# Optimization experiments

Hardware: AMD Instinct MI355X
Metric: run time of the kernel (lower is better)

## Reference

```python
import jax, jax.numpy as jnp
import numpy as np

B, N, D, O, L = 16, 2000, 128, 64, 3  # batch, n_nodes, hidden_dim, output_dim, n_layers


def _init(key, shape, fan_in):
    return jax.random.normal(key, shape, jnp.float32) / np.sqrt(fan_in).astype(np.float32)


def setup_inputs() -> dict:
    key = jax.random.key(0)
    ks = jax.random.split(key, 8)
    return {
        "coords": jax.random.normal(ks[0], (B, N, 2), jnp.float32),
        "enc_w0": _init(ks[1], (2, D), 2),
        "enc_b0": jnp.zeros((D,), jnp.float32),
        "enc_w1": _init(ks[2], (D, D), D),
        "enc_b1": jnp.zeros((D,), jnp.float32),
        "gat_W": _init(ks[3], (L, D, D), D),      # per-layer GAT projection (no bias)
        "gat_a1": _init(ks[4], (L, D), 2 * D),    # first half of attention vector a
        "gat_a2": _init(ks[5], (L, D), 2 * D),    # second half of attention vector a
        "proj_w": _init(ks[6], (D, O), D),
        "proj_b": jnp.zeros((O,), jnp.float32),
    }


def _leaky(x):
    return jnp.where(x >= 0, x, 0.2 * x)  # LeakyReLU(0.2)


def reference(coords, enc_w0, enc_b0, enc_w1, enc_b1, gat_W, gat_a1, gat_a2, proj_w, proj_b):
    # node encoder: Linear -> ReLU -> Linear
    h = jax.nn.relu(coords @ enc_w0 + enc_b0) @ enc_w1 + enc_b1  # [B,N,D]
    n_layers = gat_W.shape[0]
    for l in range(n_layers):
        Wh = h @ gat_W[l]                      # [B,N,D]
        # additive GAT attention: e_ij = leakyrelu(a1.Wh_i + a2.Wh_j)
        # (equivalent to a([Wh_i || Wh_j]) without materializing N*N*2D tensor)
        e1 = Wh @ gat_a1[l]                    # [B,N]
        e2 = Wh @ gat_a2[l]                    # [B,N]
        e = _leaky(e1[:, :, None] + e2[:, None, :])  # [B,N,N]
        # adj is all-ones in forward() so the masked_fill is a no-op
        att = jax.nn.softmax(e, axis=-1)       # [B,N,N]; dropout is identity (eval)
        h = jax.nn.relu(att @ Wh)              # [B,N,D]
    return h @ proj_w + proj_b                 # [B,N,O]
```

## Files before the change

### kernel.cpp

```cpp
#include <hip/hip_runtime.h>
#include <hip/hip_bf16.h>

using bf16 = __hip_bfloat16;

#define BATCH 16
#define NNODE 2000
#define DIM   128
#define ODIM  64
#define NLAYER 3
#define BN    (BATCH*NNODE)
#define NP1   (NNODE+1)
#define CHK   125
#define CKS   16

#define OFF_COORDS 0
#define OFF_EW0    64000
#define OFF_EB0    64256
#define OFF_EW1    64384
#define OFF_EB1    80768
#define OFF_GW     80896
#define OFF_GA1    130048
#define OFF_GA2    130432
#define OFF_PW     130816
#define OFF_PB     139008
#define CVT_TOT    139072

#define PK_GAT(l)  (32768 + (l)*32768)
#define PK_PROJ    131072
#define PK_TOT     147456

typedef __attribute__((ext_vector_type(8))) short bf16x8;
typedef __attribute__((ext_vector_type(4))) float f32x4;

__device__ __forceinline__ unsigned short f2bf(float f){
    union { float f; unsigned u; } x; x.f = f;
    unsigned r = (x.u + 0x7FFFu + ((x.u >> 16) & 1u)) >> 16;
    return (unsigned short)r;
}
__device__ __forceinline__ float bf2f(unsigned short h){
    union { unsigned u; float f; } x; x.u = ((unsigned)h) << 16;
    return x.f;
}
__device__ __forceinline__ unsigned ordu(float f){
    union { float f; unsigned u; } x; x.f = f;
    return (x.u & 0x80000000u) ? ~x.u : (x.u | 0x80000000u);
}
__device__ __forceinline__ float iordu(unsigned u){
    union { unsigned u; float f; } x;
    x.u = (u & 0x80000000u) ? (u ^ 0x80000000u) : ~u;
    return x.f;
}

struct InPtrs { const void* p[10]; };

__global__ void convert_all_k(InPtrs in, float* __restrict__ dst, float* __restrict__ flag)
{
    __shared__ int scnt[256];
    const unsigned short* raw = (const unsigned short*)in.p[0];
    int t = threadIdx.x, c = 0;
    for (int k = t; k < 2048; k += 256){
        unsigned short u = raw[2*k];
        int e = (u >> 7) & 0xFF;
        if (e >= 100 && e <= 140) ++c;
    }
    scnt[t] = c;
    __syncthreads();
    for (int s = 128; s; s >>= 1){ if (t < s) scnt[t] += scnt[t+s]; __syncthreads(); }
    const bool isbf16 = (scnt[0] >= 1800);
    if (blockIdx.x == 0 && t == 0) flag[0] = isbf16 ? 1.0f : 0.0f;

    const int off[11] = {OFF_COORDS,OFF_EW0,OFF_EB0,OFF_EW1,OFF_EB1,
                         OFF_GW,OFF_GA1,OFF_GA2,OFF_PW,OFF_PB,CVT_TOT};
    int i = blockIdx.x*256 + t;
    if (i >= CVT_TOT) return;
    int seg = 0;
    #pragma unroll
    for (int s = 1; s < 10; ++s) if (i >= off[s]) seg = s;
    int li = i - off[seg];
    if (isbf16) dst[i] = __bfloat162float(((const bf16*)in.p[seg])[li]);
    else        dst[i] = ((const float*)in.p[seg])[li];
}

__global__ __launch_bounds__(256) void prep_k(const float* __restrict__ cvt,
                                              unsigned short* __restrict__ pk,
                                              float* __restrict__ wa)
{
    const int mi = blockIdx.x, t = threadIdx.x;
    if (mi < 3){
        const float* W; unsigned short* dst; int N;
        if (mi == 0)      { W = cvt + OFF_GW + 1*DIM*DIM;  dst = pk + PK_GAT(1); N = 128; }
        else if (mi == 1) { W = cvt + OFF_GW + 2*DIM*DIM;  dst = pk + PK_GAT(2); N = 128; }
        else              { W = cvt + OFF_PW;              dst = pk + PK_PROJ;   N = 64;  }
        const int tot = 128*N;
        unsigned short* dh = dst;
        unsigned short* dl = dst + tot;
        for (int e = t; e < tot; e += 256){
            int col = e >> 7, k = e & 127;
            float v = W[k*N + col];
            unsigned short hb = f2bf(v);
            unsigned short lb = f2bf(v - bf2f(hb));
            dh[e] = hb;
            dl[e] = lb;
        }
    } else {
        for (int idx = t; idx < 3*256; idx += 256){
            const int l = idx >> 8, rem = idx & 255, half = rem >> 7, r = rem & 127;
            const float* W  = cvt + OFF_GW + l*DIM*DIM;
            const float* av = cvt + (half ? OFF_GA2 : OFF_GA1) + l*DIM;
            float s = 0.f;
            for (int c2 = 0; c2 < 128; ++c2) s = fmaf(W[r*128 + c2], av[c2], s);
            wa[l*256 + half*128 + r] = s;
        }
    }
}

__global__ __launch_bounds__(128) void prep2_k(const float* __restrict__ cvt,
    unsigned short* __restrict__ pk, const float* __restrict__ wa,
    float* __restrict__ u12, float* __restrict__ bfuse, float* __restrict__ su)
{
    const int b = blockIdx.x, t = threadIdx.x;
    const float* w1 = cvt + OFF_EW1;
    const float* W0 = cvt + OFF_GW;
    if (b < 128){
        float acc = 0.f;
        for (int d = 0; d < 128; ++d) acc = fmaf(w1[b*DIM + d], W0[d*DIM + t], acc);
        unsigned short hb = f2bf(acc), lb = f2bf(acc - bf2f(hb));
        unsigned short* dst = pk + PK_GAT(0);
        dst[t*128 + b]         = hb;
        dst[16384 + t*128 + b] = lb;
    } else if (b == 128){
        const float* b1 = cvt + OFF_EB1;
        float acc = 0.f;
        for (int d = 0; d < 128; ++d) acc = fmaf(b1[d], W0[d*DIM + t], acc);
        bfuse[t] = acc;
        if (t < 2){
            float s = 0.f;
            for (int d = 0; d < 128; ++d) s = fmaf(b1[d], wa[t*128 + d], s);
            su[t] = s;
        }
    } else {
        float a1 = 0.f, a2 = 0.f;
        for (int d = 0; d < 128; ++d){
            float w = w1[t*DIM + d];
            a1 = fmaf(w, wa[d],       a1);
            a2 = fmaf(w, wa[128 + d], a2);
        }
        u12[t]       = a1;
        u12[128 + t] = a2;
    }
}


__global__ __launch_bounds__(256) void gat0mfma_k(const float* __restrict__ cvt,
    const unsigned short* __restrict__ pk, const float* __restrict__ u12,
    const float* __restrict__ su, const float* __restrict__ bfuse,
    float* __restrict__ Wh, float* __restrict__ e1p, float* __restrict__ e2p)
{
    __shared__ unsigned short sAh[64*128], sAl[64*128];
    const int t = threadIdx.x, r0 = blockIdx.x*64;
    const int wv = t >> 6, l = t & 63, lc = l & 15, lk = l >> 4;
    const unsigned short* ph = pk;
    const unsigned short* pl = pk + 16384;
    bf16x8 bh[2][4], bl[2][4];
    #pragma unroll
    for (int cg = 0; cg < 2; ++cg){
        const int col = wv*32 + cg*16 + lc;
        #pragma unroll
        for (int kc = 0; kc < 4; ++kc){
            const int k0 = kc*32 + lk*8;
            bh[cg][kc] = *(const bf16x8*)&ph[col*128 + k0];
            bl[cg][kc] = *(const bf16x8*)&pl[col*128 + k0];
        }
    }
    const int row = t >> 2, g = t & 3;
    const float* coords = cvt + OFF_COORDS;
    const float* w0  = cvt + OFF_EW0;
    const float* b0v = cvt + OFF_EB0;
    const int node = r0 + row;
    const float c0 = coords[2*node], c1 = coords[2*node+1];
    char* shb = (char*)sAh; char* slb = (char*)sAl;
    const int swz = (row & 7) << 4;
    float e1 = 0.f, e2 = 0.f;
    #pragma unroll
    for (int i = 0; i < 8; ++i){
        const int ch = g + i*4, k0 = ch*4;
        float4 wa0 = *(const float4*)&w0[k0];
        float4 wb0 = *(const float4*)&w0[DIM + k0];
        float4 bq  = *(const float4*)&b0v[k0];
        float4 v;
        v.x = fmaf(c0, wa0.x, fmaf(c1, wb0.x, bq.x)); v.x = v.x > 0.f ? v.x : 0.f;
        v.y = fmaf(c0, wa0.y, fmaf(c1, wb0.y, bq.y)); v.y = v.y > 0.f ? v.y : 0.f;
        v.z = fmaf(c0, wa0.z, fmaf(c1, wb0.z, bq.z)); v.z = v.z > 0.f ? v.z : 0.f;
        v.w = fmaf(c0, wa0.w, fmaf(c1, wb0.w, bq.w)); v.w = v.w > 0.f ? v.w : 0.f;
        float4 q1 = *(const float4*)&u12[k0];
        float4 q2 = *(const float4*)&u12[128 + k0];
        e1 = fmaf(v.x,q1.x, fmaf(v.y,q1.y, fmaf(v.z,q1.z, fmaf(v.w,q1.w, e1))));
        e2 = fmaf(v.x,q2.x, fmaf(v.y,q2.y, fmaf(v.z,q2.z, fmaf(v.w,q2.w, e2))));
        ushort4 hq, lq;
        hq.x = f2bf(v.x); lq.x = f2bf(v.x - bf2f(hq.x));
        hq.y = f2bf(v.y); lq.y = f2bf(v.y - bf2f(hq.y));
        hq.z = f2bf(v.z); lq.z = f2bf(v.z - bf2f(hq.z));
        hq.w = f2bf(v.w); lq.w = f2bf(v.w - bf2f(hq.w));
        const int bo = (ch*8) ^ swz;
        *(ushort4*)(shb + row*256 + bo) = hq;
        *(ushort4*)(slb + row*256 + bo) = lq;
    }
    e1 += __shfl_xor(e1, 1); e1 += __shfl_xor(e1, 2);
    e2 += __shfl_xor(e2, 1); e2 += __shfl_xor(e2, 2);
    if (g == 0){ e1p[r0 + row] = e1 + su[0]; e2p[r0 + row] = e2 + su[1]; }
    __syncthreads();
    f32x4 acc[4][2] = {};
    #pragma unroll
    for (int m = 0; m < 4; ++m){
        const int ar = m*16 + lc, asw = (ar & 7) << 4;
        #pragma unroll
        for (int kc = 0; kc < 4; ++kc){
            const int bo = (kc*64 + lk*16) ^ asw;
            bf16x8 ah = *(bf16x8*)(shb + ar*256 + bo);
            bf16x8 al = *(bf16x8*)(slb + ar*256 + bo);
            #pragma unroll
            for (int cg = 0; cg < 2; ++cg){
                acc[m][cg] = __builtin_amdgcn_mfma_f32_16x16x32_bf16(ah, bh[cg][kc], acc[m][cg], 0, 0, 0);
                acc[m][cg] = __builtin_amdgcn_mfma_f32_16x16x32_bf16(ah, bl[cg][kc], acc[m][cg], 0, 0, 0);
                acc[m][cg] = __builtin_amdgcn_mfma_f32_16x16x32_bf16(al, bh[cg][kc], acc[m][cg], 0, 0, 0);
            }
        }
    }
    #pragma unroll
    for (int m = 0; m < 4; ++m){
        const int rg = r0 + m*16 + lk*4;
        #pragma unroll
        for (int cg = 0; cg < 2; ++cg){
            const int col = wv*32 + cg*16 + lc;
            const float bb = bfuse[col];
            #pragma unroll
            for (int j = 0; j < 4; ++j) Wh[(size_t)(rg+j)*DIM + col] = acc[m][cg][j] + bb;
        }
    }
}

__global__ __launch_bounds__(256) void gatmfma_k(const float* __restrict__ A,
    const unsigned short* __restrict__ pk, const float* __restrict__ wa,
    float* __restrict__ Wh, float* __restrict__ e1p, float* __restrict__ e2p)
{
    __shared__ unsigned short sAh[64*128], sAl[64*128];
    const int t = threadIdx.x, r0 = blockIdx.x*64;
    const int wv = t >> 6, l = t & 63, lc = l & 15, lk = l >> 4;
    const unsigned short* ph = pk;
    const unsigned short* pl = pk + 16384;
    bf16x8 bh[2][4], bl[2][4];
    #pragma unroll
    for (int cg = 0; cg < 2; ++cg){
        const int col = wv*32 + cg*16 + lc;
        #pragma unroll
        for (int kc = 0; kc < 4; ++kc){
            const int k0 = kc*32 + lk*8;
            bh[cg][kc] = *(const bf16x8*)&ph[col*128 + k0];
            bl[cg][kc] = *(const bf16x8*)&pl[col*128 + k0];
        }
    }
    const int row = t >> 2, g = t & 3;
    const float* Ar = A + (size_t)(r0 + row)*DIM;
    char* shb = (char*)sAh; char* slb = (char*)sAl;
    const int swz = (row & 7) << 4;
    float e1 = 0.f, e2 = 0.f;
    #pragma unroll
    for (int i = 0; i < 8; ++i){
        const int ch = g + i*4;
        float4 a  = *(const float4*)&Ar[ch*4];
        float4 u1 = *(const float4*)&wa[ch*4];
        float4 u2 = *(const float4*)&wa[128 + ch*4];
        e1 = fmaf(a.x,u1.x, fmaf(a.y,u1.y, fmaf(a.z,u1.z, fmaf(a.w,u1.w, e1))));
        e2 = fmaf(a.x,u2.x, fmaf(a.y,u2.y, fmaf(a.z,u2.z, fmaf(a.w,u2.w, e2))));
        ushort4 hq, lq;
        hq.x = f2bf(a.x); lq.x = f2bf(a.x - bf2f(hq.x));
        hq.y = f2bf(a.y); lq.y = f2bf(a.y - bf2f(hq.y));
        hq.z = f2bf(a.z); lq.z = f2bf(a.z - bf2f(hq.z));
        hq.w = f2bf(a.w); lq.w = f2bf(a.w - bf2f(hq.w));
        const int bo = (ch*8) ^ swz;
        *(ushort4*)(shb + row*256 + bo) = hq;
        *(ushort4*)(slb + row*256 + bo) = lq;
    }
    e1 += __shfl_xor(e1, 1); e1 += __shfl_xor(e1, 2);
    e2 += __shfl_xor(e2, 1); e2 += __shfl_xor(e2, 2);
    if (g == 0){ e1p[r0 + row] = e1; e2p[r0 + row] = e2; }
    __syncthreads();
    f32x4 acc[4][2] = {};
    #pragma unroll
    for (int m = 0; m < 4; ++m){
        const int ar = m*16 + lc, asw = (ar & 7) << 4;
        #pragma unroll
        for (int kc = 0; kc < 4; ++kc){
            const int bo = (kc*64 + lk*16) ^ asw;
            bf16x8 ah = *(bf16x8*)(shb + ar*256 + bo);
            bf16x8 al = *(bf16x8*)(slb + ar*256 + bo);
            #pragma unroll
            for (int cg = 0; cg < 2; ++cg){
                acc[m][cg] = __builtin_amdgcn_mfma_f32_16x16x32_bf16(ah, bh[cg][kc], acc[m][cg], 0, 0, 0);
                acc[m][cg] = __builtin_amdgcn_mfma_f32_16x16x32_bf16(ah, bl[cg][kc], acc[m][cg], 0, 0, 0);
                acc[m][cg] = __builtin_amdgcn_mfma_f32_16x16x32_bf16(al, bh[cg][kc], acc[m][cg], 0, 0, 0);
            }
        }
    }
    #pragma unroll
    for (int m = 0; m < 4; ++m){
        const int rg = r0 + m*16 + lk*4;
        #pragma unroll
        for (int cg = 0; cg < 2; ++cg){
            const int col = wv*32 + cg*16 + lc;
            #pragma unroll
            for (int j = 0; j < 4; ++j) Wh[(size_t)(rg+j)*DIM + col] = acc[m][cg][j];
        }
    }
}

__global__ __launch_bounds__(256) void projmfma_k(const float* __restrict__ A,
    const unsigned short* __restrict__ pk, const float* __restrict__ bias,
    void* __restrict__ outp, const float* __restrict__ flag)
{
    __shared__ unsigned short sAh[64*128], sAl[64*128];
    const int t = threadIdx.x, r0 = blockIdx.x*64;
    const int wv = t >> 6, l = t & 63, lc = l & 15, lk = l >> 4;
    const unsigned short* ph = pk;
    const unsigned short* pl = pk + 8192;
    bf16x8 bh[4], bl[4];
    const int col = wv*16 + lc;
    #pragma unroll
    for (int kc = 0; kc < 4; ++kc){
        const int k0 = kc*32 + lk*8;
        bh[kc] = *(const bf16x8*)&ph[col*128 + k0];
        bl[kc] = *(const bf16x8*)&pl[col*128 + k0];
    }
    const int row = t >> 2, g = t & 3;
    const float* Ar = A + (size_t)(r0 + row)*DIM;
    char* shb = (char*)sAh; char* slb = (char*)sAl;
    const int swz = (row & 7) << 4;
    #pragma unroll
    for (int i = 0; i < 8; ++i){
        const int ch = g + i*4;
        float4 a = *(const float4*)&Ar[ch*4];
        ushort4 hq, lq;
        hq.x = f2bf(a.x); lq.x = f2bf(a.x - bf2f(hq.x));
        hq.y = f2bf(a.y); lq.y = f2bf(a.y - bf2f(hq.y));
        hq.z = f2bf(a.z); lq.z = f2bf(a.z - bf2f(hq.z));
        hq.w = f2bf(a.w); lq.w = f2bf(a.w - bf2f(hq.w));
        const int bo = (ch*8) ^ swz;
        *(ushort4*)(shb + row*256 + bo) = hq;
        *(ushort4*)(slb + row*256 + bo) = lq;
    }
    __syncthreads();
    f32x4 acc[4] = {};
    #pragma unroll
    for (int m = 0; m < 4; ++m){
        const int ar = m*16 + lc, asw = (ar & 7) << 4;
        #pragma unroll
        for (int kc = 0; kc < 4; ++kc){
            const int bo = (kc*64 + lk*16) ^ asw;
            bf16x8 ah = *(bf16x8*)(shb + ar*256 + bo);
            bf16x8 al = *(bf16x8*)(slb + ar*256 + bo);
            acc[m] = __builtin_amdgcn_mfma_f32_16x16x32_bf16(ah, bh[kc], acc[m], 0, 0, 0);
            acc[m] = __builtin_amdgcn_mfma_f32_16x16x32_bf16(ah, bl[kc], acc[m], 0, 0, 0);
            acc[m] = __builtin_amdgcn_mfma_f32_16x16x32_bf16(al, bh[kc], acc[m], 0, 0, 0);
        }
    }
    const float bb = bias[col];
    const bool isbf = (flag[0] != 0.0f);
    #pragma unroll
    for (int m = 0; m < 4; ++m){
        const int rg = r0 + m*16 + lk*4;
        #pragma unroll
        for (int j = 0; j < 4; ++j){
            float v = acc[m][j] + bb;
            size_t p = (size_t)(rg+j)*ODIM + col;
            if (isbf) ((bf16*)outp)[p] = __float2bfloat16(v);
            else      ((float*)outp)[p] = v;
        }
    }
}

#define WAVE_FENCE() __asm__ volatile("" ::: "memory")
__global__ void sort_k(const float* __restrict__ e2p, float* __restrict__ e2s, int* __restrict__ sidx,
                       float* __restrict__ wp, float* __restrict__ wn, float* __restrict__ e2m)
{
    __shared__ unsigned long long kv[2048];
    const int b = blockIdx.x, t = threadIdx.x;
    for (int i = t; i < 2048; i += 1024)
        kv[i] = (i < NNODE) ? (((unsigned long long)ordu(e2p[b*NNODE + i]) << 32) | (unsigned)i)
                            : 0xFFFFFFFFFFFFFFFFull;
    __syncthreads();

    #pragma unroll 1
    for (int size = 2; size <= 128; size <<= 1){
        #pragma unroll 1
        for (int stride = size >> 1; stride > 0; stride >>= 1){
            int i = 2*t - (t & (stride-1));
            int j = i + stride;
            bool asc = ((i & size) == 0);
            unsigned long long ki = kv[i], kj = kv[j];
            bool sw = asc ? (ki > kj) : (ki < kj);
            if (sw){ kv[i] = kj; kv[j] = ki; }
            WAVE_FENCE();
        }
    }
    __syncthreads();

    #pragma unroll 1
    for (int size = 256; size <= 2048; size <<= 1){
        #pragma unroll 1
        for (int stride = size >> 1; stride >= 128; stride >>= 1){
            int i = 2*t - (t & (stride-1));
            int j = i + stride;
            bool asc = ((i & size) == 0);
            unsigned long long ki = kv[i], kj = kv[j];
            bool sw = asc ? (ki > kj) : (ki < kj);
            if (sw){ kv[i] = kj; kv[j] = ki; }
            __syncthreads();
        }
        #pragma unroll 1
        for (int stride = 64; stride > 0; stride >>= 1){
            int i = 2*t - (t & (stride-1));
            int j = i + stride;
            bool asc = ((i & size) == 0);
            unsigned long long ki = kv[i], kj = kv[j];
            bool sw = asc ? (ki > kj) : (ki < kj);
            if (sw){ kv[i] = kj; kv[j] = ki; }
            WAVE_FENCE();
        }
        __syncthreads();
    }

    const float mx = iordu((unsigned)(kv[NNODE-1] >> 32));
    for (int i = t; i < NNODE; i += 1024){
        unsigned long long key = kv[i];
        float val = iordu((unsigned)(key >> 32));
        e2s [b*NNODE+i] = val;
        sidx[b*NNODE+i] = (int)(key & 0xFFFFFFFFull);
        wp  [b*NNODE+i] = __expf(val - mx);
        wn  [b*NNODE+i] = __expf(0.2f*(val - mx));
    }
    if (t == 0) e2m[b] = mx;
}

__global__ void passA_k(const float* __restrict__ Wh, const int* __restrict__ sidx,
    const float* __restrict__ wp, const float* __restrict__ wn,
    float* __restrict__ chunkP, float* __restrict__ chunkN,
    float* __restrict__ schunkP, float* __restrict__ schunkN)
{
    const int b = blockIdx.x / CHK, c = blockIdx.x % CHK, d = threadIdx.x;
    const int base = b*NNODE;
    float sp=0.f, sn=0.f, ssp=0.f, ssn=0.f;
    #pragma unroll 4
    for (int r = c*CKS; r < c*CKS + CKS; ++r){
        int j = sidx[base + r];
        float whv = Wh[((size_t)base + j)*DIM + d];
        float wpv = wp[base + r], wnv = wn[base + r];
        sp = fmaf(wpv, whv, sp);  sn = fmaf(wnv, whv, sn);
        ssp += wpv;  ssn += wnv;
    }
    const int idx = b*CHK + c;
    chunkP[idx*DIM + d] = sp;
    chunkN[idx*DIM + d] = sn;
    if (d == 0){ schunkP[idx] = ssp; schunkN[idx] = ssn; }
}

__global__ __launch_bounds__(256) void passB_k(
    const float* __restrict__ chunkP, const float* __restrict__ chunkN,
    const float* __restrict__ schunkP, const float* __restrict__ schunkN,
    float* __restrict__ offP, float* __restrict__ offN,
    float* __restrict__ soffP, float* __restrict__ soffN)
{
    const int b = blockIdx.x, tid = threadIdx.x;
    const bool doP = (blockIdx.y == 0);
    const float* chunk  = doP ? chunkP  : chunkN;
    const float* schunk = doP ? schunkP : schunkN;
    float* off  = doP ? offP  : offN;
    float* soff = doP ? soffP : soffN;

    if (tid < 128){
        const int d = tid;
        float acc = 0.f, v[25];
        #pragma unroll
        for (int t = 0; t < 5; ++t){
            const int c0 = doP ? (4-t)*25 : t*25;
            #pragma unroll
            for (int k = 0; k < 25; ++k) v[k] = chunk[(b*CHK + c0 + k)*DIM + d];
            if (doP){
                #pragma unroll
                for (int k = 24; k >= 0; --k){ off[(b*CHK + c0 + k)*DIM + d] = acc; acc += v[k]; }
            } else {
                #pragma unroll
                for (int k = 0; k < 25; ++k){ off[(b*CHK + c0 + k)*DIM + d] = acc; acc += v[k]; }
            }
        }
    } else if (tid == 128){
        float sacc = 0.f, sv[25];
        #pragma unroll
        for (int t = 0; t < 5; ++t){
            const int c0 = doP ? (4-t)*25 : t*25;
            #pragma unroll
            for (int k = 0; k < 25; ++k) sv[k] = schunk[b*CHK + c0 + k];
            if (doP){
                #pragma unroll
                for (int k = 24; k >= 0; --k){ soff[b*CHK + c0 + k] = sacc; sacc += sv[k]; }
            } else {
                #pragma unroll
                for (int k = 0; k < 25; ++k){ soff[b*CHK + c0 + k] = sacc; sacc += sv[k]; }
            }
        }
    }
}

__global__ void passC_k(const float* __restrict__ Wh, const int* __restrict__ sidx,
    const float* __restrict__ wp, const float* __restrict__ wn,
    const float* __restrict__ offP, const float* __restrict__ offN,
    const float* __restrict__ soffP, const float* __restrict__ soffN,
    float* __restrict__ Ppos, float* __restrict__ Pneg,
    float* __restrict__ pposs, float* __restrict__ pnegs)
{
    const int b = blockIdx.x / CHK, c = blockIdx.x % CHK, d = threadIdx.x;
    const int base = b*NNODE;
    const size_t pb = (size_t)b*NP1;
    const int idx = b*CHK + c;
    const int r0 = c*CKS, r1 = r0 + CKS;

    if (c == CHK-1){
        Ppos[(pb + NNODE)*DIM + d] = 0.f;
        if (d == 0) pposs[pb + NNODE] = 0.f;
    }
    float pr = offP[idx*DIM + d], spr = soffP[idx];
    for (int r = r1-1; r >= r0; --r){
        int j = sidx[base + r];
        float whv = Wh[((size_t)base + j)*DIM + d];
        float wpv = wp[base + r];
        pr  = fmaf(wpv, whv, pr);
        spr += wpv;
        Ppos[(pb + r)*DIM + d] = pr;
        if (d == 0) pposs[pb + r] = spr;
    }
    float nr = offN[idx*DIM + d], snr = soffN[idx];
    for (int r = r0; r < r1; ++r){
        int j = sidx[base + r];
        float whv = Wh[((size_t)base + j)*DIM + d];
        float wnv = wn[base + r];
        Pneg[(pb + r)*DIM + d] = nr;
        if (d == 0) pnegs[pb + r] = snr;
        nr  = fmaf(wnv, whv, nr);
        snr += wnv;
    }
    if (c == CHK-1){
        Pneg[(pb + NNODE)*DIM + d] = nr;
        if (d == 0) pnegs[pb + NNODE] = snr;
    }
}

__global__ __launch_bounds__(128) void out16_k(const float* __restrict__ e1p,
    const float* __restrict__ e2s, const float* __restrict__ e2m,
    const float* __restrict__ Ppos, const float* __restrict__ Pneg,
    const float* __restrict__ pposs, const float* __restrict__ pnegs, float* __restrict__ h)
{
    __shared__ int   slo[CKS];
    __shared__ float sps[CKS], sns[CKS];
    const int b = blockIdx.x / CHK, c = blockIdx.x % CHK, d = threadIdx.x;
    const int base = b*NNODE, r0 = c*CKS;
    const size_t pb = (size_t)b*NP1;

    if (d < CKS){
        int row = base + r0 + d;
        float e1v = e1p[row];
        float s = e1v + e2m[b];
        float m = (s >= 0.f) ? s : 0.2f*s;
        sps[d] = __expf(s - m);
        sns[d] = __expf(0.2f*s - m);
        const float* es = e2s + base;
        float tt = -e1v;
        int lo = 0, hi = NNODE;
        while (lo < hi){ int mid = (lo+hi) >> 1; if (es[mid] < tt) lo = mid+1; else hi = mid; }
        slo[d] = lo;
    }
    __syncthreads();
    #pragma unroll 4
    for (int k = 0; k < CKS; ++k){
        int row = base + r0 + k;
        size_t kb = pb + slo[k];
        float numer = sps[k]*Ppos[kb*DIM + d] + sns[k]*Pneg[kb*DIM + d];
        float Z     = sps[k]*pposs[kb]        + sns[k]*pnegs[kb];
        float q = numer / Z;
        h[(size_t)row*DIM + d] = (q > 0.f) ? q : ((q == q) ? 0.f : q);
    }
}

extern "C" void kernel_launch(void* const* d_in, const int* in_sizes, int n_in,
                              void* d_out, int out_size, void* d_ws, size_t ws_size,
                              hipStream_t stream)
{
    (void)in_sizes; (void)n_in; (void)out_size; (void)ws_size;

    float* f = (float*)d_ws;
    float* flag    = f;  f += 4;
    float* cvt     = f;  f += CVT_TOT;
    float* h       = f;  f += (size_t)BN*DIM;
    float* Wh      = f;  f += (size_t)BN*DIM;
    float* Ppos    = f;  f += (size_t)BATCH*NP1*DIM;
    float* Pneg    = f;  f += (size_t)BATCH*NP1*DIM;
    float* chunkP  = f;  f += BATCH*CHK*DIM;
    float* chunkN  = f;  f += BATCH*CHK*DIM;
    float* offP    = f;  f += BATCH*CHK*DIM;
    float* offN    = f;  f += BATCH*CHK*DIM;
    float* schunkP = f;  f += BATCH*CHK;
    float* schunkN = f;  f += BATCH*CHK;
    float* soffP   = f;  f += BATCH*CHK;
    float* soffN   = f;  f += BATCH*CHK;
    float* e1p     = f;  f += BN;
    float* e2p     = f;  f += BN;
    float* e2s     = f;  f += BN;
    float* wp      = f;  f += BN;
    float* wn      = f;  f += BN;
    float* pposs   = f;  f += BATCH*NP1;
    float* pnegs   = f;  f += BATCH*NP1;
    float* e2m     = f;  f += 16;
    int*   sidx    = (int*)f;
    unsigned short* pk = (unsigned short*)(sidx + BN);
    float* wa      = (float*)(pk + PK_TOT);
    float* u12     = wa + 768;
    float* bfuse   = u12 + 256;
    float* su      = bfuse + 128;

    InPtrs ip;
    for (int i = 0; i < 10; ++i) ip.p[i] = d_in[i];
    convert_all_k<<<(CVT_TOT+255)/256, 256, 0, stream>>>(ip, cvt, flag);

    prep_k<<<4, 256, 0, stream>>>(cvt, pk, wa);
    prep2_k<<<130, 128, 0, stream>>>(cvt, pk, wa, u12, bfuse, su);

    for (int l = 0; l < NLAYER; ++l){
        if (l == 0)
            gat0mfma_k<<<BN/64, 256, 0, stream>>>(cvt, pk + PK_GAT(0), u12, su, bfuse,
                                                  Wh, e1p, e2p);
        else
            gatmfma_k<<<BN/64, 256, 0, stream>>>(h, pk + PK_GAT(l), wa + l*256, Wh, e1p, e2p);
        sort_k<<<BATCH, 1024, 0, stream>>>(e2p, e2s, sidx, wp, wn, e2m);
        passA_k<<<BATCH*CHK, DIM, 0, stream>>>(Wh, sidx, wp, wn, chunkP, chunkN, schunkP, schunkN);
        passB_k<<<dim3(BATCH, 2), 256, 0, stream>>>(chunkP, chunkN, schunkP, schunkN,
                                                    offP, offN, soffP, soffN);
        passC_k<<<BATCH*CHK, DIM, 0, stream>>>(Wh, sidx, wp, wn, offP, offN, soffP, soffN,
                                               Ppos, Pneg, pposs, pnegs);
        out16_k<<<BATCH*CHK, DIM, 0, stream>>>(e1p, e2s, e2m, Ppos, Pneg, pposs, pnegs, h);
    }

    projmfma_k<<<BN/64, 256, 0, stream>>>(h, pk + PK_PROJ, cvt + OFF_PB, d_out, flag);
}
```

Measured before the change: 301.9 us.

## Merge chunk-sum and local prefix passes, apply chunk offsets in output kernel

The chunked prefix-sum scheme previously read the gathered Wh rows twice, once in passA for chunk totals and again in passC for the offset-adjusted prefixes. Now a single pass writes chunk-local prefix sums along with the chunk totals. The output kernel adds the cross-chunk offset from passB at lookup time. This drops one kernel launch per layer and one full gather over Wh, at the cost of two extra offset reads per output row in the final kernel.

```diff
diff --git a/kernel.cpp b/kernel.cpp
--- a/kernel.cpp
+++ b/kernel.cpp
@@ -441,26 +441,52 @@
     if (t == 0) e2m[b] = mx;
 }
 
-__global__ void passA_k(const float* __restrict__ Wh, const int* __restrict__ sidx,
+__global__ void passAC_k(const float* __restrict__ Wh, const int* __restrict__ sidx,
     const float* __restrict__ wp, const float* __restrict__ wn,
+    float* __restrict__ localP, float* __restrict__ localN,
+    float* __restrict__ lposs, float* __restrict__ lnegs,
     float* __restrict__ chunkP, float* __restrict__ chunkN,
     float* __restrict__ schunkP, float* __restrict__ schunkN)
 {
     const int b = blockIdx.x / CHK, c = blockIdx.x % CHK, d = threadIdx.x;
     const int base = b*NNODE;
-    float sp=0.f, sn=0.f, ssp=0.f, ssn=0.f;
-    #pragma unroll 4
-    for (int r = c*CKS; r < c*CKS + CKS; ++r){
+    const size_t pb = (size_t)b*NP1;
+    const int idx = b*CHK + c;
+    const int r0 = c*CKS, r1 = r0 + CKS;
+
+    if (c == CHK-1){
+        localP[(pb + NNODE)*DIM + d] = 0.f;
+        if (d == 0) lposs[pb + NNODE] = 0.f;
+    }
+    float pr = 0.f, spr = 0.f;
+    for (int r = r1-1; r >= r0; --r){
         int j = sidx[base + r];
         float whv = Wh[((size_t)base + j)*DIM + d];
-        float wpv = wp[base + r], wnv = wn[base + r];
-        sp = fmaf(wpv, whv, sp);  sn = fmaf(wnv, whv, sn);
-        ssp += wpv;  ssn += wnv;
-    }
-    const int idx = b*CHK + c;
-    chunkP[idx*DIM + d] = sp;
-    chunkN[idx*DIM + d] = sn;
-    if (d == 0){ schunkP[idx] = ssp; schunkN[idx] = ssn; }
+        float wpv = wp[base + r];
+        pr  = fmaf(wpv, whv, pr);
+        spr += wpv;
+        localP[(pb + r)*DIM + d] = pr;
+        if (d == 0) lposs[pb + r] = spr;
+    }
+    chunkP[idx*DIM + d] = pr;
+    if (d == 0) schunkP[idx] = spr;
+
+    float nr = 0.f, snr = 0.f;
+    for (int r = r0; r < r1; ++r){
+        int j = sidx[base + r];
+        float whv = Wh[((size_t)base + j)*DIM + d];
+        float wnv = wn[base + r];
+        localN[(pb + r)*DIM + d] = nr;
+        if (d == 0) lnegs[pb + r] = snr;
+        nr  = fmaf(wnv, whv, nr);
+        snr += wnv;
+    }
+    if (c == CHK-1){
+        localN[(pb + NNODE)*DIM + d] = nr;
+        if (d == 0) lnegs[pb + NNODE] = snr;
+    }
+    chunkN[idx*DIM + d] = nr;
+    if (d == 0) schunkN[idx] = snr;
 }
 
 __global__ __launch_bounds__(256) void passB_k(
@@ -510,53 +536,13 @@
     }
 }
 
-__global__ void passC_k(const float* __restrict__ Wh, const int* __restrict__ sidx,
-    const float* __restrict__ wp, const float* __restrict__ wn,
+__global__ __launch_bounds__(128) void out16f_k(const float* __restrict__ e1p,
+    const float* __restrict__ e2s, const float* __restrict__ e2m,
+    const float* __restrict__ localP, const float* __restrict__ localN,
+    const float* __restrict__ lposs, const float* __restrict__ lnegs,
     const float* __restrict__ offP, const float* __restrict__ offN,
     const float* __restrict__ soffP, const float* __restrict__ soffN,
-    float* __restrict__ Ppos, float* __restrict__ Pneg,
-    float* __restrict__ pposs, float* __restrict__ pnegs)
-{
-    const int b = blockIdx.x / CHK, c = blockIdx.x % CHK, d = threadIdx.x;
-    const int base = b*NNODE;
-    const size_t pb = (size_t)b*NP1;
-    const int idx = b*CHK + c;
-    const int r0 = c*CKS, r1 = r0 + CKS;
-
-    if (c == CHK-1){
-        Ppos[(pb + NNODE)*DIM + d] = 0.f;
-        if (d == 0) pposs[pb + NNODE] = 0.f;
-    }
-    float pr = offP[idx*DIM + d], spr = soffP[idx];
-    for (int r = r1-1; r >= r0; --r){
-        int j = sidx[base + r];
-        float whv = Wh[((size_t)base + j)*DIM + d];
-        float wpv = wp[base + r];
-        pr  = fmaf(wpv, whv, pr);
-        spr += wpv;
-        Ppos[(pb + r)*DIM + d] = pr;
-        if (d == 0) pposs[pb + r] = spr;
-    }
-    float nr = offN[idx*DIM + d], snr = soffN[idx];
-    for (int r = r0; r < r1; ++r){
-        int j = sidx[base + r];
-        float whv = Wh[((size_t)base + j)*DIM + d];
-        float wnv = wn[base + r];
-        Pneg[(pb + r)*DIM + d] = nr;
-        if (d == 0) pnegs[pb + r] = snr;
-        nr  = fmaf(wnv, whv, nr);
-        snr += wnv;
-    }
-    if (c == CHK-1){
-        Pneg[(pb + NNODE)*DIM + d] = nr;
-        if (d == 0) pnegs[pb + NNODE] = snr;
-    }
-}
-
-__global__ __launch_bounds__(128) void out16_k(const float* __restrict__ e1p,
-    const float* __restrict__ e2s, const float* __restrict__ e2m,
-    const float* __restrict__ Ppos, const float* __restrict__ Pneg,
-    const float* __restrict__ pposs, const float* __restrict__ pnegs, float* __restrict__ h)
+    float* __restrict__ h)
 {
     __shared__ int   slo[CKS];
     __shared__ float sps[CKS], sns[CKS];
@@ -581,9 +567,14 @@
     #pragma unroll 4
     for (int k = 0; k < CKS; ++k){
         int row = base + r0 + k;
-        size_t kb = pb + slo[k];
-        float numer = sps[k]*Ppos[kb*DIM + d] + sns[k]*Pneg[kb*DIM + d];
-        float Z     = sps[k]*pposs[kb]        + sns[k]*pnegs[kb];
+        int lo = slo[k];
+        int cl = lo >> 4; if (cl > CHK-1) cl = CHK-1;
+        size_t kb = pb + lo;
+        int ob = b*CHK + cl;
+        float pP = localP[kb*DIM + d] + offP[(size_t)ob*DIM + d];
+        float pN = localN[kb*DIM + d] + offN[(size_t)ob*DIM + d];
+        float numer = sps[k]*pP + sns[k]*pN;
+        float Z     = sps[k]*(lposs[kb] + soffP[ob]) + sns[k]*(lnegs[kb] + soffN[ob]);
         float q = numer / Z;
         h[(size_t)row*DIM + d] = (q > 0.f) ? q : ((q == q) ? 0.f : q);
     }
@@ -639,12 +630,12 @@
         else
             gatmfma_k<<<BN/64, 256, 0, stream>>>(h, pk + PK_GAT(l), wa + l*256, Wh, e1p, e2p);
         sort_k<<<BATCH, 1024, 0, stream>>>(e2p, e2s, sidx, wp, wn, e2m);
-        passA_k<<<BATCH*CHK, DIM, 0, stream>>>(Wh, sidx, wp, wn, chunkP, chunkN, schunkP, schunkN);
+        passAC_k<<<BATCH*CHK, DIM, 0, stream>>>(Wh, sidx, wp, wn, Ppos, Pneg, pposs, pnegs,
+                                                chunkP, chunkN, schunkP, schunkN);
         passB_k<<<dim3(BATCH, 2), 256, 0, stream>>>(chunkP, chunkN, schunkP, schunkN,
                                                     offP, offN, soffP, soffN);
-        passC_k<<<BATCH*CHK, DIM, 0, stream>>>(Wh, sidx, wp, wn, offP, offN, soffP, soffN,
-                                               Ppos, Pneg, pposs, pnegs);
-        out16_k<<<BATCH*CHK, DIM, 0, stream>>>(e1p, e2s, e2m, Ppos, Pneg, pposs, pnegs, h);
+        out16f_k<<<BATCH*CHK, DIM, 0, stream>>>(e1p, e2s, e2m, Ppos, Pneg, pposs, pnegs,
+                                                offP, offN, soffP, soffN, h);
     }
 
     projmfma_k<<<BN/64, 256, 0, stream>>>(h, pk + PK_PROJ, cvt + OFF_PB, d_out, flag);
```

New measurement: 294.8 us. 2.3% less time.

## Bucket query rows by split point and fuse prefix scan with attention output

Applied to the files above, without the earlier changes.

The sort kernel now also computes each query row's split point and exp scale factors, then counting-sorts rows into buckets keyed by split index. A fused output kernel recomputes chunk offsets directly, walks each chunk's sorted keys in reverse, and writes outputs for rows whose split falls there. This removes the full Ppos/Pneg prefix arrays (16×2001×128×2 floats) and two kernel launches per layer. In exchange, each block redundantly sums up to 125 chunk partials, and per-row work is imbalanced across blocks because bucket sizes vary.

```diff
diff --git a/kernel.cpp b/kernel.cpp
--- a/kernel.cpp
+++ b/kernel.cpp
@@ -12,6 +12,7 @@
 #define NP1   (NNODE+1)
 #define CHK   125
 #define CKS   16
+#define NOFF  2002
 
 #define OFF_COORDS 0
 #define OFF_EW0    64000
@@ -379,10 +380,14 @@
 }
 
 #define WAVE_FENCE() __asm__ volatile("" ::: "memory")
-__global__ void sort_k(const float* __restrict__ e2p, float* __restrict__ e2s, int* __restrict__ sidx,
-                       float* __restrict__ wp, float* __restrict__ wn, float* __restrict__ e2m)
+__global__ void sortE_k(const float* __restrict__ e2p, const float* __restrict__ e1p,
+    int* __restrict__ sidx, float* __restrict__ wp, float* __restrict__ wn,
+    float* __restrict__ sps, float* __restrict__ sns,
+    int* __restrict__ bucketRow, int* __restrict__ bucketOff)
 {
     __shared__ unsigned long long kv[2048];
+    __shared__ int cnt[NOFF];
+    __shared__ int ofs[NOFF];
     const int b = blockIdx.x, t = threadIdx.x;
     for (int i = t; i < 2048; i += 1024)
         kv[i] = (i < NNODE) ? (((unsigned long long)ordu(e2p[b*NNODE + i]) << 32) | (unsigned)i)
@@ -433,15 +438,65 @@
     for (int i = t; i < NNODE; i += 1024){
         unsigned long long key = kv[i];
         float val = iordu((unsigned)(key >> 32));
-        e2s [b*NNODE+i] = val;
         sidx[b*NNODE+i] = (int)(key & 0xFFFFFFFFull);
         wp  [b*NNODE+i] = __expf(val - mx);
         wn  [b*NNODE+i] = __expf(0.2f*(val - mx));
     }
-    if (t == 0) e2m[b] = mx;
-}
-
-__global__ void passA_k(const float* __restrict__ Wh, const int* __restrict__ sidx,
+    for (int i = t; i < NOFF; i += 1024) cnt[i] = 0;
+    __syncthreads();
+
+    int loA[2] = {-1, -1};
+    #pragma unroll
+    for (int q = 0; q < 2; ++q){
+        const int i = t + q*1024;
+        if (i < NNODE){
+            float e1v = e1p[b*NNODE + i];
+            float s = e1v + mx;
+            float m = (s >= 0.f) ? s : 0.2f*s;
+            sps[b*NNODE + i] = __expf(s - m);
+            sns[b*NNODE + i] = __expf(0.2f*s - m);
+            unsigned tt = ordu(-e1v);
+            int lo = 0, hi = NNODE;
+            while (lo < hi){
+                int mid = (lo + hi) >> 1;
+                if ((unsigned)(kv[mid] >> 32) < tt) lo = mid + 1; else hi = mid;
+            }
+            loA[q] = lo;
+            atomicAdd(&cnt[lo], 1);
+        }
+    }
+    __syncthreads();
+
+    if (t < 64){
+        const int b0 = t*32;
+        int s = 0;
+        for (int k = 0; k < 32; ++k){ int id = b0+k; if (id < NOFF) s += cnt[id]; }
+        int inc = s;
+        #pragma unroll
+        for (int d2 = 1; d2 < 64; d2 <<= 1){
+            int v = __shfl_up(inc, d2);
+            if (t >= d2) inc += v;
+        }
+        int run = inc - s;
+        for (int k = 0; k < 32; ++k){ int id = b0+k; if (id < NOFF){ ofs[id] = run; run += cnt[id]; } }
+    }
+    __syncthreads();
+    for (int i = t; i < NOFF; i += 1024){
+        bucketOff[b*NOFF + i] = ofs[i];
+        cnt[i] = ofs[i];
+    }
+    __syncthreads();
+    #pragma unroll
+    for (int q = 0; q < 2; ++q){
+        const int i = t + q*1024;
+        if (i < NNODE){
+            int pos = atomicAdd(&cnt[loA[q]], 1);
+            bucketRow[b*NNODE + pos] = i;
+        }
+    }
+}
+
+__global__ void chunkSums_k(const float* __restrict__ Wh, const int* __restrict__ sidx,
     const float* __restrict__ wp, const float* __restrict__ wn,
     float* __restrict__ chunkP, float* __restrict__ chunkN,
     float* __restrict__ schunkP, float* __restrict__ schunkN)
@@ -463,129 +518,70 @@
     if (d == 0){ schunkP[idx] = ssp; schunkN[idx] = ssn; }
 }
 
-__global__ __launch_bounds__(256) void passB_k(
+__global__ __launch_bounds__(128) void outFused_k(const float* __restrict__ Wh,
+    const int* __restrict__ sidx, const float* __restrict__ wp, const float* __restrict__ wn,
     const float* __restrict__ chunkP, const float* __restrict__ chunkN,
     const float* __restrict__ schunkP, const float* __restrict__ schunkN,
-    float* __restrict__ offP, float* __restrict__ offN,
-    float* __restrict__ soffP, float* __restrict__ soffN)
-{
-    const int b = blockIdx.x, tid = threadIdx.x;
-    const bool doP = (blockIdx.y == 0);
-    const float* chunk  = doP ? chunkP  : chunkN;
-    const float* schunk = doP ? schunkP : schunkN;
-    float* off  = doP ? offP  : offN;
-    float* soff = doP ? soffP : soffN;
-
-    if (tid < 128){
-        const int d = tid;
-        float acc = 0.f, v[25];
-        #pragma unroll
-        for (int t = 0; t < 5; ++t){
-            const int c0 = doP ? (4-t)*25 : t*25;
-            #pragma unroll
-            for (int k = 0; k < 25; ++k) v[k] = chunk[(b*CHK + c0 + k)*DIM + d];
-            if (doP){
-                #pragma unroll
-                for (int k = 24; k >= 0; --k){ off[(b*CHK + c0 + k)*DIM + d] = acc; acc += v[k]; }
-            } else {
-                #pragma unroll
-                for (int k = 0; k < 25; ++k){ off[(b*CHK + c0 + k)*DIM + d] = acc; acc += v[k]; }
-            }
-        }
-    } else if (tid == 128){
-        float sacc = 0.f, sv[25];
-        #pragma unroll
-        for (int t = 0; t < 5; ++t){
-            const int c0 = doP ? (4-t)*25 : t*25;
-            #pragma unroll
-            for (int k = 0; k < 25; ++k) sv[k] = schunk[b*CHK + c0 + k];
-            if (doP){
-                #pragma unroll
-                for (int k = 24; k >= 0; --k){ soff[b*CHK + c0 + k] = sacc; sacc += sv[k]; }
-            } else {
-                #pragma unroll
-                for (int k = 0; k < 25; ++k){ soff[b*CHK + c0 + k] = sacc; sacc += sv[k]; }
-            }
-        }
-    }
-}
-
-__global__ void passC_k(const float* __restrict__ Wh, const int* __restrict__ sidx,
-    const float* __restrict__ wp, const float* __restrict__ wn,
-    const float* __restrict__ offP, const float* __restrict__ offN,
-    const float* __restrict__ soffP, const float* __restrict__ soffN,
-    float* __restrict__ Ppos, float* __restrict__ Pneg,
-    float* __restrict__ pposs, float* __restrict__ pnegs)
-{
-    const int b = blockIdx.x / CHK, c = blockIdx.x % CHK, d = threadIdx.x;
-    const int base = b*NNODE;
-    const size_t pb = (size_t)b*NP1;
-    const int idx = b*CHK + c;
-    const int r0 = c*CKS, r1 = r0 + CKS;
-
-    if (c == CHK-1){
-        Ppos[(pb + NNODE)*DIM + d] = 0.f;
-        if (d == 0) pposs[pb + NNODE] = 0.f;
-    }
-    float pr = offP[idx*DIM + d], spr = soffP[idx];
-    for (int r = r1-1; r >= r0; --r){
-        int j = sidx[base + r];
-        float whv = Wh[((size_t)base + j)*DIM + d];
-        float wpv = wp[base + r];
-        pr  = fmaf(wpv, whv, pr);
-        spr += wpv;
-        Ppos[(pb + r)*DIM + d] = pr;
-        if (d == 0) pposs[pb + r] = spr;
-    }
-    float nr = offN[idx*DIM + d], snr = soffN[idx];
-    for (int r = r0; r < r1; ++r){
-        int j = sidx[base + r];
-        float whv = Wh[((size_t)base + j)*DIM + d];
-        float wnv = wn[base + r];
-        Pneg[(pb + r)*DIM + d] = nr;
-        if (d == 0) pnegs[pb + r] = snr;
-        nr  = fmaf(wnv, whv, nr);
-        snr += wnv;
-    }
-    if (c == CHK-1){
-        Pneg[(pb + NNODE)*DIM + d] = nr;
-        if (d == 0) pnegs[pb + NNODE] = snr;
-    }
-}
-
-__global__ __launch_bounds__(128) void out16_k(const float* __restrict__ e1p,
-    const float* __restrict__ e2s, const float* __restrict__ e2m,
-    const float* __restrict__ Ppos, const float* __restrict__ Pneg,
-    const float* __restrict__ pposs, const float* __restrict__ pnegs, float* __restrict__ h)
-{
-    __shared__ int   slo[CKS];
-    __shared__ float sps[CKS], sns[CKS];
+    const int* __restrict__ bucketRow, const int* __restrict__ bucketOff,
+    const float* __restrict__ sps, const float* __restrict__ sns,
+    float* __restrict__ h)
+{
     const int b = blockIdx.x / CHK, c = blockIdx.x % CHK, d = threadIdx.x;
     const int base = b*NNODE, r0 = c*CKS;
-    const size_t pb = (size_t)b*NP1;
-
-    if (d < CKS){
-        int row = base + r0 + d;
-        float e1v = e1p[row];
-        float s = e1v + e2m[b];
-        float m = (s >= 0.f) ? s : 0.2f*s;
-        sps[d] = __expf(s - m);
-        sns[d] = __expf(0.2f*s - m);
-        const float* es = e2s + base;
-        float tt = -e1v;
-        int lo = 0, hi = NNODE;
-        while (lo < hi){ int mid = (lo+hi) >> 1; if (es[mid] < tt) lo = mid+1; else hi = mid; }
-        slo[d] = lo;
-    }
-    __syncthreads();
-    #pragma unroll 4
-    for (int k = 0; k < CKS; ++k){
-        int row = base + r0 + k;
-        size_t kb = pb + slo[k];
-        float numer = sps[k]*Ppos[kb*DIM + d] + sns[k]*Pneg[kb*DIM + d];
-        float Z     = sps[k]*pposs[kb]        + sns[k]*pnegs[kb];
-        float q = numer / Z;
-        h[(size_t)row*DIM + d] = (q > 0.f) ? q : ((q == q) ? 0.f : q);
+    const int cb = b*CHK;
+
+    float offP = 0.f, soffP = 0.f;
+    for (int c2 = c+1; c2 < CHK; ++c2){
+        offP  += chunkP[(size_t)(cb + c2)*DIM + d];
+        soffP += schunkP[cb + c2];
+    }
+    float offN = 0.f, soffN = 0.f;
+    for (int c2 = 0; c2 < c; ++c2){
+        offN  += chunkN[(size_t)(cb + c2)*DIM + d];
+        soffN += schunkN[cb + c2];
+    }
+
+    float whv[CKS], wpv[CKS], wnv[CKS];
+    #pragma unroll
+    for (int r = 0; r < CKS; ++r){
+        int j = sidx[base + r0 + r];
+        whv[r] = Wh[((size_t)base + j)*DIM + d];
+        wpv[r] = wp[base + r0 + r];
+        wnv[r] = wn[base + r0 + r];
+    }
+    float totN = 0.f, totSN = 0.f;
+    #pragma unroll
+    for (int r = 0; r < CKS; ++r){ totN = fmaf(wnv[r], whv[r], totN); totSN += wnv[r]; }
+
+    const int* bo = bucketOff + b*NOFF;
+    const int* brow = bucketRow + b*NNODE;
+
+    if (c == CHK-1){
+        for (int q = bo[NNODE]; q < bo[NNODE+1]; ++q){
+            int row = brow[q];
+            float spsv = sps[base+row], snsv = sns[base+row];
+            float pP = offP;
+            float pN = totN + offN;
+            float Z  = spsv*soffP + snsv*(totSN + soffN);
+            float v  = (spsv*pP + snsv*pN) / Z;
+            h[((size_t)base+row)*DIM + d] = (v > 0.f) ? v : ((v == v) ? 0.f : v);
+        }
+    }
+    float suffP = 0.f, suffN = 0.f, suffSP = 0.f, suffSN = 0.f;
+    #pragma unroll 1
+    for (int r = CKS-1; r >= 0; --r){
+        suffP = fmaf(wpv[r], whv[r], suffP);  suffSP += wpv[r];
+        suffN = fmaf(wnv[r], whv[r], suffN);  suffSN += wnv[r];
+        const int L = r0 + r;
+        for (int q = bo[L]; q < bo[L+1]; ++q){
+            int row = brow[q];
+            float spsv = sps[base+row], snsv = sns[base+row];
+            float pP = suffP + offP;
+            float pN = (totN - suffN) + offN;
+            float Z  = spsv*(suffSP + soffP) + snsv*((totSN - suffSN) + soffN);
+            float v  = (spsv*pP + snsv*pN) / Z;
+            h[((size_t)base+row)*DIM + d] = (v > 0.f) ? v : ((v == v) ? 0.f : v);
+        }
     }
 }
 
@@ -600,26 +596,20 @@
     float* cvt     = f;  f += CVT_TOT;
     float* h       = f;  f += (size_t)BN*DIM;
     float* Wh      = f;  f += (size_t)BN*DIM;
-    float* Ppos    = f;  f += (size_t)BATCH*NP1*DIM;
-    float* Pneg    = f;  f += (size_t)BATCH*NP1*DIM;
     float* chunkP  = f;  f += BATCH*CHK*DIM;
     float* chunkN  = f;  f += BATCH*CHK*DIM;
-    float* offP    = f;  f += BATCH*CHK*DIM;
-    float* offN    = f;  f += BATCH*CHK*DIM;
     float* schunkP = f;  f += BATCH*CHK;
     float* schunkN = f;  f += BATCH*CHK;
-    float* soffP   = f;  f += BATCH*CHK;
-    float* soffN   = f;  f += BATCH*CHK;
     float* e1p     = f;  f += BN;
     float* e2p     = f;  f += BN;
-    float* e2s     = f;  f += BN;
     float* wp      = f;  f += BN;
     float* wn      = f;  f += BN;
-    float* pposs   = f;  f += BATCH*NP1;
-    float* pnegs   = f;  f += BATCH*NP1;
-    float* e2m     = f;  f += 16;
-    int*   sidx    = (int*)f;
-    unsigned short* pk = (unsigned short*)(sidx + BN);
+    float* sps     = f;  f += BN;
+    float* sns     = f;  f += BN;
+    int*   sidx      = (int*)f;              f += BN;
+    int*   bucketRow = (int*)f;              f += BN;
+    int*   bucketOff = (int*)f;              f += BATCH*NOFF;
+    unsigned short* pk = (unsigned short*)f;
     float* wa      = (float*)(pk + PK_TOT);
     float* u12     = wa + 768;
     float* bfuse   = u12 + 256;
@@ -638,13 +628,13 @@
                                                   Wh, e1p, e2p);
         else
             gatmfma_k<<<BN/64, 256, 0, stream>>>(h, pk + PK_GAT(l), wa + l*256, Wh, e1p, e2p);
-        sort_k<<<BATCH, 1024, 0, stream>>>(e2p, e2s, sidx, wp, wn, e2m);
-        passA_k<<<BATCH*CHK, DIM, 0, stream>>>(Wh, sidx, wp, wn, chunkP, chunkN, schunkP, schunkN);
-        passB_k<<<dim3(BATCH, 2), 256, 0, stream>>>(chunkP, chunkN, schunkP, schunkN,
-                                                    offP, offN, soffP, soffN);
-        passC_k<<<BATCH*CHK, DIM, 0, stream>>>(Wh, sidx, wp, wn, offP, offN, soffP, soffN,
-                                               Ppos, Pneg, pposs, pnegs);
-        out16_k<<<BATCH*CHK, DIM, 0, stream>>>(e1p, e2s, e2m, Ppos, Pneg, pposs, pnegs, h);
+        sortE_k<<<BATCH, 1024, 0, stream>>>(e2p, e1p, sidx, wp, wn, sps, sns,
+                                            bucketRow, bucketOff);
+        chunkSums_k<<<BATCH*CHK, DIM, 0, stream>>>(Wh, sidx, wp, wn,
+                                                   chunkP, chunkN, schunkP, schunkN);
+        outFused_k<<<BATCH*CHK, DIM, 0, stream>>>(Wh, sidx, wp, wn,
+                                                  chunkP, chunkN, schunkP, schunkN,
+                                                  bucketRow, bucketOff, sps, sns, h);
     }
 
     projmfma_k<<<BN/64, 256, 0, stream>>>(h, pk + PK_PROJ, cvt + OFF_PB, d_out, flag);
```

Result: slower. 894.2 us (+196.2%).
